# Kernel optimization log

Measured on AMD Instinct MI355X. Metric: run time of the kernel, lower is better.

## Reference

```python
import jax, jax.numpy as jnp
import numpy as np


def recursive_fht(x):
    # Faithful vectorized version of the module's recursive butterfly FHT
    # (twiddle = cas(2*pi*n/N), no flipped-odd term, exactly as in the source).
    N = x.shape[-1]
    if N == 1:
        return x
    e = recursive_fht(x[..., ::2])
    o = recursive_fht(x[..., 1::2])
    n = jnp.arange(N // 2, dtype=x.dtype)
    t = jnp.cos(2 * jnp.pi * n / N) + jnp.sin(2 * jnp.pi * n / N)
    return jnp.concatenate([e + t * o, e - t * o], axis=-1)


def compl_mul1d(x1, x2):
    # x1: [B, i, modes], x2: [i, o, modes]; flips along axis 0 as in the source
    x1f = x1[::-1]
    x2f = x2[::-1]
    return 0.5 * (jnp.einsum('bix,iox->box', x1, x2)
                  - jnp.einsum('bix,iox->box', x1f, x2f)
                  + jnp.einsum('bix,iox->box', x1, x2f)
                  + jnp.einsum('bix,iox->box', x1f, x2))


def idht(X):
    # Inverse discrete Hartley transform via the cas matrix (DHT is an
    # involution up to 1/K). K = N//2+1 is not a power of 2, so a dense
    # transform is used. Compute-bound batched GEMM.
    K = X.shape[-1]
    n = jnp.arange(K, dtype=X.dtype)
    ang = 2.0 * jnp.pi * jnp.outer(n, n) / K
    cas = jnp.cos(ang) + jnp.sin(ang)  # [K, K]
    return jnp.einsum('bck,kn->bcn', X, cas) / K


def setup_inputs() -> dict:
    key = jax.random.key(0)
    k1, k2 = jax.random.split(key)
    B, Cin, Cout, N, modes1 = 32, 64, 64, 4096, 1024
    x = jax.random.normal(k1, (B, Cin, N), dtype=jnp.float32)
    scale = 1.0 / (Cin * Cout)
    weights1 = scale * jax.random.uniform(k2, (Cin, Cout, modes1), dtype=jnp.float32)
    return {"x": x, "weights1": weights1, "modes1": modes1}


def reference(x, weights1, modes1):
    B, C, N = x.shape
    # dht with threshold=1.0: FHT along last axis, low-pass filter is a no-op
    x_ht = recursive_fht(x)
    K = N // 2 + 1
    out_ht = jnp.zeros((B, C, K), dtype=x.dtype)
    out_ht = out_ht.at[:, :, :modes1].set(compl_mul1d(x_ht[:, :, :modes1], weights1))
    return idht(out_ht)  # [B, C, N//2+1]
```

## Files before the change

kernel.cpp:

```cpp
#include <hip/hip_runtime.h>
#include <hip/hip_bf16.h>

#define BATCH 32
#define CIN   64
#define COUT  64
#define NFFT  4096
#define MODES 1024
#define KOUT  2049
#define NPAD  2176

typedef __bf16 bf16x8 __attribute__((ext_vector_type(8)));
typedef float  f32x4  __attribute__((ext_vector_type(4)));

#define AS1 __attribute__((address_space(1)))
#define AS3 __attribute__((address_space(3)))

static __device__ __forceinline__ void gl_lds16(const void* g, void* l) {
    __builtin_amdgcn_global_load_lds((const AS1 void*)g, (AS3 void*)l, 16, 0, 0);
}

static __device__ __forceinline__ void bfly4(float eA, float eB, float oA, float oB,
                                             float t, float c0, float c1,
                                             float& w0, float& w1, float& w2, float& w3) {
    float PA = fmaf(t, oA, eA), MA = fmaf(-t, oA, eA);
    float PB = fmaf(t, oB, eB), MB = fmaf(-t, oB, eB);
    w0 = fmaf(c0, PB, PA);
    w2 = fmaf(-c0, PB, PA);
    w1 = fmaf(c1, MB, MA);
    w3 = fmaf(-c1, MB, MA);
}


__global__ void fill_tw(float* __restrict__ tw) {
    int t = blockIdx.x * blockDim.x + threadIdx.x;
    if (t >= NFFT) return;
    if (t == 0) { tw[0] = 1.0f; return; }
    int h = 1 << (31 - __clz(t));
    int n = t - h;
    float ang = 3.14159265358979323846f * (float)n / (float)h;
    tw[t] = cosf(ang) + sinf(ang);
}

__global__ void fill_c2t(__hip_bfloat16* __restrict__ hi, __hip_bfloat16* __restrict__ lo) {
    int idx = blockIdx.x * blockDim.x + threadIdx.x;
    if (idx >= NPAD * MODES) return;
    int n = idx >> 10;
    int k = idx & 1023;
    float v = 0.0f;
    if (n < KOUT) {
        int m = (k * n) % KOUT;
        float ang = 6.28318530717958647692f * (float)m / (float)KOUT;
        v = (cosf(ang) + sinf(ang)) * (1.0f / (float)KOUT);
    }
    __hip_bfloat16 h = __float2bfloat16(v);
    hi[idx] = h;
    lo[idx] = __float2bfloat16(v - __bfloat162float(h));
}

__global__ __launch_bounds__(256) void fht_kernel(const float* __restrict__ x,
                                                  const float* __restrict__ tw,
                                                  float* __restrict__ xh) {
    __shared__ __align__(16) float bufA[NFFT];
    __shared__ __align__(16) float bufB[NFFT];
    const int tid = threadIdx.x;
    const int row = blockIdx.x;
    const float4* xr = (const float4*)(x + (size_t)row * NFFT);
    float4* bA4 = (float4*)bufA;
#pragma unroll
    for (int j = 0; j < 4; ++j) bA4[tid + j * 256] = xr[tid + j * 256];
    __syncthreads();

    float* src = bufA;
    float* dst = bufB;

#pragma unroll
    for (int p = 0; p < 3; ++p) {
        const int s = 2 * p;
        const int L = 1 << s;
        const int shift = 11 - s;
        const int hq = 1 << (shift - 1);
#pragma unroll
        for (int q = 0; q < 4; ++q) {
            const int u = tid + q * 256;
            const int kap = u >> (shift - 1);
            const int gp = u & (hq - 1);
            const int b0 = (kap << (shift + 1)) + gp;
            float eA = src[b0];
            float eB = src[b0 + hq];
            float oA = src[b0 + 2 * hq];
            float oB = src[b0 + 3 * hq];
            float t  = tw[L + kap], c0 = tw[2 * L + kap], c1 = tw[3 * L + kap];
            float w0, w1, w2, w3;
            bfly4(eA, eB, oA, oB, t, c0, c1, w0, w1, w2, w3);
            dst[u]        = w0;
            dst[u + 1024] = w1;
            dst[u + 2048] = w2;
            dst[u + 3072] = w3;
        }
        __syncthreads();
        float* tmp = src; src = dst; dst = tmp;
    }

#pragma unroll
    for (int p = 3; p < 5; ++p) {
        const int s = 2 * p;
        const int L = 1 << s;
        const int shift = 11 - s;
        const int hq = 1 << (shift - 1);
        const int u0 = 4 * tid;
        const int kap = u0 >> (shift - 1);
        const int gp = u0 & (hq - 1);
        const int b0 = (kap << (shift + 1)) + gp;
        float4 V0 = *(const float4*)(src + b0);
        float4 V1 = *(const float4*)(src + b0 + hq);
        float4 V2 = *(const float4*)(src + b0 + 2 * hq);
        float4 V3 = *(const float4*)(src + b0 + 3 * hq);
        float t  = tw[L + kap], c0 = tw[2 * L + kap], c1 = tw[3 * L + kap];
        float4 W0, W1, W2, W3;
        bfly4(V0.x, V1.x, V2.x, V3.x, t, c0, c1, W0.x, W1.x, W2.x, W3.x);
        bfly4(V0.y, V1.y, V2.y, V3.y, t, c0, c1, W0.y, W1.y, W2.y, W3.y);
        bfly4(V0.z, V1.z, V2.z, V3.z, t, c0, c1, W0.z, W1.z, W2.z, W3.z);
        bfly4(V0.w, V1.w, V2.w, V3.w, t, c0, c1, W0.w, W1.w, W2.w, W3.w);
        *(float4*)(dst + u0)        = W0;
        *(float4*)(dst + u0 + 1024) = W1;
        *(float4*)(dst + u0 + 2048) = W2;
        *(float4*)(dst + u0 + 3072) = W3;
        __syncthreads();
        float* tmp = src; src = dst; dst = tmp;
    }

    {
        const int u0 = 4 * tid;
        float4 R0 = *(const float4*)(src + 4 * u0);
        float4 R1 = *(const float4*)(src + 4 * u0 + 4);
        float4 R2 = *(const float4*)(src + 4 * u0 + 8);
        float4 R3 = *(const float4*)(src + 4 * u0 + 12);
        float4 T  = *(const float4*)(tw + 1024 + u0);
        float4 C0 = *(const float4*)(tw + 2048 + u0);
        float4 C1 = *(const float4*)(tw + 3072 + u0);
        float4 W0, W1, W2, W3;
        bfly4(R0.x, R0.y, R0.z, R0.w, T.x, C0.x, C1.x, W0.x, W1.x, W2.x, W3.x);
        bfly4(R1.x, R1.y, R1.z, R1.w, T.y, C0.y, C1.y, W0.y, W1.y, W2.y, W3.y);
        bfly4(R2.x, R2.y, R2.z, R2.w, T.z, C0.z, C1.z, W0.z, W1.z, W2.z, W3.z);
        bfly4(R3.x, R3.y, R3.z, R3.w, T.w, C0.w, C1.w, W0.w, W1.w, W2.w, W3.w);
        *(float4*)(dst + u0)        = W0;
        *(float4*)(dst + u0 + 1024) = W1;
        *(float4*)(dst + u0 + 2048) = W2;
        *(float4*)(dst + u0 + 3072) = W3;
        __syncthreads();
        float* tmp = src; src = dst; dst = tmp;
    }

    ((float4*)(xh + (size_t)row * MODES))[tid] = ((const float4*)src)[tid];
}

__global__ __launch_bounds__(256) void mix_kernel(const f32x4* __restrict__ xh,
                                                  const f32x4* __restrict__ w,
                                                  ushort4* __restrict__ y_hi) {
    const int kl = threadIdx.x & 63;
    const int jg = threadIdx.x >> 6;
    const int k4 = blockIdx.x * 64 + kl;
    const int b  = blockIdx.y;
    const int rb = (BATCH - 1) - b;
    const int o0 = blockIdx.z * 8 + jg * 2;

    f32x4 accb[2], accr[2];
#pragma unroll
    for (int j = 0; j < 2; ++j) {
        accb[j] = (f32x4){0.f, 0.f, 0.f, 0.f};
        accr[j] = (f32x4){0.f, 0.f, 0.f, 0.f};
    }

#pragma unroll 2
    for (int i = 0; i < 32; ++i) {
        const int mi = 63 - i;
        f32x4 xai = xh[(size_t)(b  * CIN + i ) * 256 + k4];
        f32x4 xam = xh[(size_t)(b  * CIN + mi) * 256 + k4];
        f32x4 xbi = xh[(size_t)(rb * CIN + i ) * 256 + k4];
        f32x4 xbm = xh[(size_t)(rb * CIN + mi) * 256 + k4];
        f32x4 w10 = w[(size_t)(i  * COUT + o0    ) * 256 + k4];
        f32x4 w20 = w[(size_t)(mi * COUT + o0    ) * 256 + k4];
        f32x4 w11 = w[(size_t)(i  * COUT + o0 + 1) * 256 + k4];
        f32x4 w21 = w[(size_t)(mi * COUT + o0 + 1) * 256 + k4];
        f32x4 sa = xai + xam;
        f32x4 da = xai - xam;
        f32x4 sb = xbi + xbm;
        f32x4 db = xbi - xbm;
        f32x4 wp0 = w10 + w20, wm0 = w10 - w20;
        f32x4 wp1 = w11 + w21, wm1 = w11 - w21;
        accb[0] += sa * wp0 + db * wm0;
        accr[0] += sb * wp0 + da * wm0;
        accb[1] += sa * wp1 + db * wm1;
        accr[1] += sb * wp1 + da * wm1;
    }

#pragma unroll
    for (int j = 0; j < 2; ++j) {
        const int o = o0 + j;
        const size_t ib = (size_t)(b  * COUT + o) * 256 + k4;
        const size_t ir = (size_t)(rb * COUT + o) * 256 + k4;
        f32x4 vb = accb[j] * 0.5f;
        f32x4 vr = accr[j] * 0.5f;
        __hip_bfloat16 b0 = __float2bfloat16(vb.x), b1 = __float2bfloat16(vb.y),
                       b2 = __float2bfloat16(vb.z), b3 = __float2bfloat16(vb.w);
        __hip_bfloat16 r0 = __float2bfloat16(vr.x), r1 = __float2bfloat16(vr.y),
                       r2 = __float2bfloat16(vr.z), r3 = __float2bfloat16(vr.w);
        y_hi[ib] = make_ushort4(*(unsigned short*)&b0, *(unsigned short*)&b1,
                                *(unsigned short*)&b2, *(unsigned short*)&b3);
        y_hi[ir] = make_ushort4(*(unsigned short*)&r0, *(unsigned short*)&r1,
                                *(unsigned short*)&r2, *(unsigned short*)&r3);
    }
}

__global__ __launch_bounds__(256) void idht_mfma(const __hip_bfloat16* __restrict__ yh,
                                                 const __hip_bfloat16* __restrict__ ch,
                                                 const __hip_bfloat16* __restrict__ cl,
                                                 float* __restrict__ out) {
    __shared__ __align__(16) char sa_h[8 * 1024];
    __shared__ __align__(16) char sb_h[4 * 1024];
    __shared__ __align__(16) char sb_l[4 * 1024];

    const int tid  = threadIdx.x;
    const int lane = tid & 63;
    const int wave = tid >> 6;
    const int wm = wave & 1;
    const int wn = wave >> 1;
    const int rbase = blockIdx.x * 128;
    const int nbase = blockIdx.y * 64;

    const int lrow = (lane & 15) * 2048;
    const int lchk = (lane >> 4) * 16;

    f32x4 acc[4][2];
#pragma unroll
    for (int mt = 0; mt < 4; ++mt)
#pragma unroll
        for (int nt = 0; nt < 2; ++nt) acc[mt][nt] = (f32x4){0.f, 0.f, 0.f, 0.f};

    for (int k0 = 0; k0 < MODES; k0 += 32) {
        const char* ga  = (const char*)yh + (size_t)rbase * 2048 + k0 * 2;
        const char* gbh = (const char*)ch + (size_t)nbase * 2048 + k0 * 2;
        const char* gbl = (const char*)cl + (size_t)nbase * 2048 + k0 * 2;

        gl_lds16(ga  + (size_t)(wave * 16) * 2048 + lrow + lchk,       sa_h + wave * 1024);
        gl_lds16(ga  + (size_t)((wave + 4) * 16) * 2048 + lrow + lchk, sa_h + (wave + 4) * 1024);
        gl_lds16(gbh + (size_t)(wave * 16) * 2048 + lrow + lchk,       sb_h + wave * 1024);
        gl_lds16(gbl + (size_t)(wave * 16) * 2048 + lrow + lchk,       sb_l + wave * 1024);
        __syncthreads();

        bf16x8 a_[4], bh_[2], bl_[2];
#pragma unroll
        for (int mt = 0; mt < 4; ++mt)
            a_[mt] = *(const bf16x8*)(sa_h + (wm * 4 + mt) * 1024 + lane * 16);
#pragma unroll
        for (int nt = 0; nt < 2; ++nt) {
            bh_[nt] = *(const bf16x8*)(sb_h + (wn * 2 + nt) * 1024 + lane * 16);
            bl_[nt] = *(const bf16x8*)(sb_l + (wn * 2 + nt) * 1024 + lane * 16);
        }
#pragma unroll
        for (int mt = 0; mt < 4; ++mt)
#pragma unroll
            for (int nt = 0; nt < 2; ++nt) {
                acc[mt][nt] = __builtin_amdgcn_mfma_f32_16x16x32_bf16(a_[mt], bh_[nt], acc[mt][nt], 0, 0, 0);
                acc[mt][nt] = __builtin_amdgcn_mfma_f32_16x16x32_bf16(a_[mt], bl_[nt], acc[mt][nt], 0, 0, 0);
            }
        __syncthreads();
    }

#pragma unroll
    for (int mt = 0; mt < 4; ++mt) {
        int row = rbase + wm * 64 + mt * 16 + (lane >> 4) * 4;
#pragma unroll
        for (int nt = 0; nt < 2; ++nt) {
            int col = nbase + wn * 32 + nt * 16 + (lane & 15);
            if (col < KOUT) {
#pragma unroll
                for (int r = 0; r < 4; ++r)
                    out[(size_t)(row + r) * KOUT + col] = acc[mt][nt][r];
            }
        }
    }
}

extern "C" void kernel_launch(void* const* d_in, const int* in_sizes, int n_in,
                              void* d_out, int out_size, void* d_ws, size_t ws_size,
                              hipStream_t stream) {
    const float* x = (const float*)d_in[0];
    const float* w = (const float*)d_in[1];
    float* out = (float*)d_out;

    float* tw = (float*)d_ws;
    float* xh = tw + NFFT;
    __hip_bfloat16* y_hi = (__hip_bfloat16*)(xh + (size_t)BATCH * CIN * MODES);
    __hip_bfloat16* c2h  = y_hi + (size_t)BATCH * COUT * MODES;
    __hip_bfloat16* c2l  = c2h + (size_t)NPAD * MODES;

    fill_tw<<<NFFT / 256, 256, 0, stream>>>(tw);
    fill_c2t<<<(NPAD * MODES + 255) / 256, 256, 0, stream>>>(c2h, c2l);
    fht_kernel<<<BATCH * CIN, 256, 0, stream>>>(x, tw, xh);
    mix_kernel<<<dim3(4, 16, 8), 256, 0, stream>>>((const f32x4*)xh, (const f32x4*)w,
                                                   (ushort4*)y_hi);
    idht_mfma<<<dim3((BATCH * COUT) / 128, NPAD / 64), 256, 0, stream>>>(y_hi, c2h, c2l, out);
}
```

Measured before the change: 170.4 us.

## Drop bf16 lo-split of cas matrix, double-buffer IDHT GEMM, simplify FHT first stage

Removes the low-order bf16 correction term of the cas matrix, halving the MFMA work and the B-matrix traffic in the IDHT GEMM. It also double-buffers the LDS staging with K=64 per step, so global-to-LDS loads overlap the MFMAs. In addition it specialises the first FHT radix-4 stage (all twiddles equal 1), makes the twiddle index wave-uniform, and halves the mix kernel's outputs per thread while doubling its grid. Dropping the lo term lowers the accuracy of the IDHT, which may push the error against the fp32 reference past tolerance.

```diff
diff --git a/kernel.cpp b/kernel.cpp
--- a/kernel.cpp
+++ b/kernel.cpp
@@ -41,7 +41,7 @@
     tw[t] = cosf(ang) + sinf(ang);
 }
 
-__global__ void fill_c2t(__hip_bfloat16* __restrict__ hi, __hip_bfloat16* __restrict__ lo) {
+__global__ void fill_c2t(__hip_bfloat16* __restrict__ hi) {
     int idx = blockIdx.x * blockDim.x + threadIdx.x;
     if (idx >= NPAD * MODES) return;
     int n = idx >> 10;
@@ -52,9 +52,7 @@
         float ang = 6.28318530717958647692f * (float)m / (float)KOUT;
         v = (cosf(ang) + sinf(ang)) * (1.0f / (float)KOUT);
     }
-    __hip_bfloat16 h = __float2bfloat16(v);
-    hi[idx] = h;
-    lo[idx] = __float2bfloat16(v - __bfloat162float(h));
+    hi[idx] = __float2bfloat16(v);
 }
 
 __global__ __launch_bounds__(256) void fht_kernel(const float* __restrict__ x,
@@ -73,8 +71,27 @@
     float* src = bufA;
     float* dst = bufB;
 
-#pragma unroll
-    for (int p = 0; p < 3; ++p) {
+    {
+#pragma unroll
+        for (int q = 0; q < 4; ++q) {
+            const int u = tid + q * 256;
+            float eA = src[u];
+            float eB = src[u + 1024];
+            float oA = src[u + 2048];
+            float oB = src[u + 3072];
+            float PA = eA + oA, MA = eA - oA;
+            float PB = eB + oB, MB = eB - oB;
+            dst[u]        = PA + PB;
+            dst[u + 2048] = PA - PB;
+            dst[u + 1024] = MA + MB;
+            dst[u + 3072] = MA - MB;
+        }
+        __syncthreads();
+        float* tmp = src; src = dst; dst = tmp;
+    }
+
+#pragma unroll
+    for (int p = 1; p < 3; ++p) {
         const int s = 2 * p;
         const int L = 1 << s;
         const int shift = 11 - s;
@@ -82,7 +99,7 @@
 #pragma unroll
         for (int q = 0; q < 4; ++q) {
             const int u = tid + q * 256;
-            const int kap = u >> (shift - 1);
+            const int kap = __builtin_amdgcn_readfirstlane(u >> (shift - 1));
             const int gp = u & (hq - 1);
             const int b0 = (kap << (shift + 1)) + gp;
             float eA = src[b0];
@@ -162,63 +179,48 @@
     const int k4 = blockIdx.x * 64 + kl;
     const int b  = blockIdx.y;
     const int rb = (BATCH - 1) - b;
-    const int o0 = blockIdx.z * 8 + jg * 2;
-
-    f32x4 accb[2], accr[2];
-#pragma unroll
-    for (int j = 0; j < 2; ++j) {
-        accb[j] = (f32x4){0.f, 0.f, 0.f, 0.f};
-        accr[j] = (f32x4){0.f, 0.f, 0.f, 0.f};
-    }
-
-#pragma unroll 2
+    const int o  = blockIdx.z * 4 + jg;
+
+    f32x4 accb = (f32x4){0.f, 0.f, 0.f, 0.f};
+    f32x4 accr = (f32x4){0.f, 0.f, 0.f, 0.f};
+
+#pragma unroll 4
     for (int i = 0; i < 32; ++i) {
         const int mi = 63 - i;
         f32x4 xai = xh[(size_t)(b  * CIN + i ) * 256 + k4];
         f32x4 xam = xh[(size_t)(b  * CIN + mi) * 256 + k4];
         f32x4 xbi = xh[(size_t)(rb * CIN + i ) * 256 + k4];
         f32x4 xbm = xh[(size_t)(rb * CIN + mi) * 256 + k4];
-        f32x4 w10 = w[(size_t)(i  * COUT + o0    ) * 256 + k4];
-        f32x4 w20 = w[(size_t)(mi * COUT + o0    ) * 256 + k4];
-        f32x4 w11 = w[(size_t)(i  * COUT + o0 + 1) * 256 + k4];
-        f32x4 w21 = w[(size_t)(mi * COUT + o0 + 1) * 256 + k4];
+        f32x4 w1 = w[(size_t)(i  * COUT + o) * 256 + k4];
+        f32x4 w2 = w[(size_t)(mi * COUT + o) * 256 + k4];
         f32x4 sa = xai + xam;
         f32x4 da = xai - xam;
         f32x4 sb = xbi + xbm;
         f32x4 db = xbi - xbm;
-        f32x4 wp0 = w10 + w20, wm0 = w10 - w20;
-        f32x4 wp1 = w11 + w21, wm1 = w11 - w21;
-        accb[0] += sa * wp0 + db * wm0;
-        accr[0] += sb * wp0 + da * wm0;
-        accb[1] += sa * wp1 + db * wm1;
-        accr[1] += sb * wp1 + da * wm1;
-    }
-
-#pragma unroll
-    for (int j = 0; j < 2; ++j) {
-        const int o = o0 + j;
-        const size_t ib = (size_t)(b  * COUT + o) * 256 + k4;
-        const size_t ir = (size_t)(rb * COUT + o) * 256 + k4;
-        f32x4 vb = accb[j] * 0.5f;
-        f32x4 vr = accr[j] * 0.5f;
-        __hip_bfloat16 b0 = __float2bfloat16(vb.x), b1 = __float2bfloat16(vb.y),
-                       b2 = __float2bfloat16(vb.z), b3 = __float2bfloat16(vb.w);
-        __hip_bfloat16 r0 = __float2bfloat16(vr.x), r1 = __float2bfloat16(vr.y),
-                       r2 = __float2bfloat16(vr.z), r3 = __float2bfloat16(vr.w);
-        y_hi[ib] = make_ushort4(*(unsigned short*)&b0, *(unsigned short*)&b1,
-                                *(unsigned short*)&b2, *(unsigned short*)&b3);
-        y_hi[ir] = make_ushort4(*(unsigned short*)&r0, *(unsigned short*)&r1,
-                                *(unsigned short*)&r2, *(unsigned short*)&r3);
-    }
+        f32x4 wp = w1 + w2, wm = w1 - w2;
+        accb += sa * wp + db * wm;
+        accr += sb * wp + da * wm;
+    }
+
+    const size_t ib = (size_t)(b  * COUT + o) * 256 + k4;
+    const size_t ir = (size_t)(rb * COUT + o) * 256 + k4;
+    f32x4 vb = accb * 0.5f;
+    f32x4 vr = accr * 0.5f;
+    __hip_bfloat16 b0 = __float2bfloat16(vb.x), b1 = __float2bfloat16(vb.y),
+                   b2 = __float2bfloat16(vb.z), b3 = __float2bfloat16(vb.w);
+    __hip_bfloat16 r0 = __float2bfloat16(vr.x), r1 = __float2bfloat16(vr.y),
+                   r2 = __float2bfloat16(vr.z), r3 = __float2bfloat16(vr.w);
+    y_hi[ib] = make_ushort4(*(unsigned short*)&b0, *(unsigned short*)&b1,
+                            *(unsigned short*)&b2, *(unsigned short*)&b3);
+    y_hi[ir] = make_ushort4(*(unsigned short*)&r0, *(unsigned short*)&r1,
+                            *(unsigned short*)&r2, *(unsigned short*)&r3);
 }
 
 __global__ __launch_bounds__(256) void idht_mfma(const __hip_bfloat16* __restrict__ yh,
                                                  const __hip_bfloat16* __restrict__ ch,
-                                                 const __hip_bfloat16* __restrict__ cl,
                                                  float* __restrict__ out) {
-    __shared__ __align__(16) char sa_h[8 * 1024];
-    __shared__ __align__(16) char sb_h[4 * 1024];
-    __shared__ __align__(16) char sb_l[4 * 1024];
+    __shared__ __align__(16) char sa[2][16 * 1024];
+    __shared__ __align__(16) char sb[2][8 * 1024];
 
     const int tid  = threadIdx.x;
     const int lane = tid & 63;
@@ -231,40 +233,51 @@
     const int lrow = (lane & 15) * 2048;
     const int lchk = (lane >> 4) * 16;
 
+    const char* ga  = (const char*)yh + (size_t)rbase * 2048;
+    const char* gbh = (const char*)ch + (size_t)nbase * 2048;
+
     f32x4 acc[4][2];
 #pragma unroll
     for (int mt = 0; mt < 4; ++mt)
 #pragma unroll
         for (int nt = 0; nt < 2; ++nt) acc[mt][nt] = (f32x4){0.f, 0.f, 0.f, 0.f};
 
-    for (int k0 = 0; k0 < MODES; k0 += 32) {
-        const char* ga  = (const char*)yh + (size_t)rbase * 2048 + k0 * 2;
-        const char* gbh = (const char*)ch + (size_t)nbase * 2048 + k0 * 2;
-        const char* gbl = (const char*)cl + (size_t)nbase * 2048 + k0 * 2;
-
-        gl_lds16(ga  + (size_t)(wave * 16) * 2048 + lrow + lchk,       sa_h + wave * 1024);
-        gl_lds16(ga  + (size_t)((wave + 4) * 16) * 2048 + lrow + lchk, sa_h + (wave + 4) * 1024);
-        gl_lds16(gbh + (size_t)(wave * 16) * 2048 + lrow + lchk,       sb_h + wave * 1024);
-        gl_lds16(gbl + (size_t)(wave * 16) * 2048 + lrow + lchk,       sb_l + wave * 1024);
-        __syncthreads();
-
-        bf16x8 a_[4], bh_[2], bl_[2];
-#pragma unroll
-        for (int mt = 0; mt < 4; ++mt)
-            a_[mt] = *(const bf16x8*)(sa_h + (wm * 4 + mt) * 1024 + lane * 16);
-#pragma unroll
-        for (int nt = 0; nt < 2; ++nt) {
-            bh_[nt] = *(const bf16x8*)(sb_h + (wn * 2 + nt) * 1024 + lane * 16);
-            bl_[nt] = *(const bf16x8*)(sb_l + (wn * 2 + nt) * 1024 + lane * 16);
-        }
-#pragma unroll
-        for (int mt = 0; mt < 4; ++mt)
-#pragma unroll
-            for (int nt = 0; nt < 2; ++nt) {
-                acc[mt][nt] = __builtin_amdgcn_mfma_f32_16x16x32_bf16(a_[mt], bh_[nt], acc[mt][nt], 0, 0, 0);
-                acc[mt][nt] = __builtin_amdgcn_mfma_f32_16x16x32_bf16(a_[mt], bl_[nt], acc[mt][nt], 0, 0, 0);
-            }
-        __syncthreads();
+    auto stage = [&](int bi, int k0) {
+#pragma unroll
+        for (int r = 0; r < 4; ++r) {
+            int ab = wave + r * 4;
+            gl_lds16(ga + (size_t)(ab >> 1) * 32768 + lrow + (ab & 1) * 64 + lchk + k0 * 2,
+                     sa[bi] + ab * 1024);
+        }
+#pragma unroll
+        for (int r = 0; r < 2; ++r) {
+            int bb = wave + r * 4;
+            gl_lds16(gbh + (size_t)(bb >> 1) * 32768 + lrow + (bb & 1) * 64 + lchk + k0 * 2,
+                     sb[bi] + bb * 1024);
+        }
+    };
+
+    stage(0, 0);
+    int cur = 0;
+    for (int ks = 0; ks < MODES / 64; ++ks) {
+        __syncthreads();
+        if (ks + 1 < MODES / 64) stage(1 - cur, (ks + 1) * 64);
+#pragma unroll
+        for (int kc = 0; kc < 2; ++kc) {
+            bf16x8 a_[4], b_[2];
+#pragma unroll
+            for (int mt = 0; mt < 4; ++mt)
+                a_[mt] = *(const bf16x8*)(sa[cur] + ((wm * 4 + mt) * 2 + kc) * 1024 + lane * 16);
+#pragma unroll
+            for (int nt = 0; nt < 2; ++nt)
+                b_[nt] = *(const bf16x8*)(sb[cur] + ((wn * 2 + nt) * 2 + kc) * 1024 + lane * 16);
+#pragma unroll
+            for (int mt = 0; mt < 4; ++mt)
+#pragma unroll
+                for (int nt = 0; nt < 2; ++nt)
+                    acc[mt][nt] = __builtin_amdgcn_mfma_f32_16x16x32_bf16(a_[mt], b_[nt], acc[mt][nt], 0, 0, 0);
+        }
+        cur ^= 1;
     }
 
 #pragma unroll
@@ -293,12 +306,11 @@
     float* xh = tw + NFFT;
     __hip_bfloat16* y_hi = (__hip_bfloat16*)(xh + (size_t)BATCH * CIN * MODES);
     __hip_bfloat16* c2h  = y_hi + (size_t)BATCH * COUT * MODES;
-    __hip_bfloat16* c2l  = c2h + (size_t)NPAD * MODES;
 
     fill_tw<<<NFFT / 256, 256, 0, stream>>>(tw);
-    fill_c2t<<<(NPAD * MODES + 255) / 256, 256, 0, stream>>>(c2h, c2l);
+    fill_c2t<<<(NPAD * MODES + 255) / 256, 256, 0, stream>>>(c2h);
     fht_kernel<<<BATCH * CIN, 256, 0, stream>>>(x, tw, xh);
-    mix_kernel<<<dim3(4, 16, 8), 256, 0, stream>>>((const f32x4*)xh, (const f32x4*)w,
-                                                   (ushort4*)y_hi);
-    idht_mfma<<<dim3((BATCH * COUT) / 128, NPAD / 64), 256, 0, stream>>>(y_hi, c2h, c2l, out);
-}
+    mix_kernel<<<dim3(4, 16, 16), 256, 0, stream>>>((const f32x4*)xh, (const f32x4*)w,
+                                                    (ushort4*)y_hi);
+    idht_mfma<<<dim3((BATCH * COUT) / 128, NPAD / 64), 256, 0, stream>>>(y_hi, c2h, out);
+}
```

After: 164.6 us. 3.4% less time.
